# Performance work log

Hardware: AMD Instinct MI355X
Metric: run time of the kernel (lower is better)

Reference implementation:

```python
import jax, jax.numpy as jnp
import numpy as np

N_NODES = 50000
N_EDGES = 1600000
NODE_DIM = 16
EDGE_DIM = 16
PIPE_F = 4
HID = 64
L = 3


def _lin(k, fan_in, fan_out):
    kw, kb = jax.random.split(k)
    bound = 1.0 / np.sqrt(fan_in)
    w = jax.random.uniform(kw, (fan_in, fan_out), jnp.float32, -bound, bound)
    b = jax.random.uniform(kb, (fan_out,), jnp.float32, -bound, bound)
    return w, b


def setup_inputs() -> dict:
    key = jax.random.key(0)
    ks = jax.random.split(key, 16)
    leak_area = jax.random.normal(ks[0], (N_NODES, 1), jnp.float32)
    pipe_attrs = jax.random.normal(ks[1], (N_EDGES, PIPE_F), jnp.float32)
    edge_index = jax.random.randint(ks[2], (2, N_EDGES), 0, N_NODES, jnp.int32)
    node_embed_w, node_embed_b = _lin(ks[3], 1, NODE_DIM)
    edge_embed_w, edge_embed_b = _lin(ks[4], PIPE_F, EDGE_DIM)
    # per-layer MLP params, stacked along leading layer axis
    ew1, eb1, ew2, eb2, nw1, nb1, nw2, nb2 = [], [], [], [], [], [], [], []
    for l in range(L):
        kl = jax.random.fold_in(ks[5], l)
        k1, k2, k3, k4 = jax.random.split(kl, 4)
        w, b = _lin(k1, 2 * NODE_DIM + EDGE_DIM, HID); ew1.append(w); eb1.append(b)
        w, b = _lin(k2, HID, EDGE_DIM); ew2.append(w); eb2.append(b)
        w, b = _lin(k3, NODE_DIM + EDGE_DIM, HID); nw1.append(w); nb1.append(b)
        w, b = _lin(k4, HID, NODE_DIM); nw2.append(w); nb2.append(b)
    final_node_w, final_node_b = _lin(ks[6], NODE_DIM, 1)
    final_edge_w, final_edge_b = _lin(ks[7], EDGE_DIM, 1)
    return {
        "leak_area": leak_area,
        "pipe_attrs": pipe_attrs,
        "edge_index": edge_index,
        "node_embed_w": node_embed_w, "node_embed_b": node_embed_b,
        "edge_embed_w": edge_embed_w, "edge_embed_b": edge_embed_b,
        "edge_mlp_w1": jnp.stack(ew1), "edge_mlp_b1": jnp.stack(eb1),
        "edge_mlp_w2": jnp.stack(ew2), "edge_mlp_b2": jnp.stack(eb2),
        "node_mlp_w1": jnp.stack(nw1), "node_mlp_b1": jnp.stack(nb1),
        "node_mlp_w2": jnp.stack(nw2), "node_mlp_b2": jnp.stack(nb2),
        "final_node_w": final_node_w, "final_node_b": final_node_b,
        "final_edge_w": final_edge_w, "final_edge_b": final_edge_b,
    }


def reference(leak_area, pipe_attrs, edge_index,
              node_embed_w, node_embed_b, edge_embed_w, edge_embed_b,
              edge_mlp_w1, edge_mlp_b1, edge_mlp_w2, edge_mlp_b2,
              node_mlp_w1, node_mlp_b1, node_mlp_w2, node_mlp_b2,
              final_node_w, final_node_b, final_edge_w, final_edge_b):
    x = leak_area @ node_embed_w + node_embed_b          # [N, node_dim]
    e = pipe_attrs @ edge_embed_w + edge_embed_b          # [E, edge_dim]
    src = edge_index[0]  # x_j (source, PyG default flow source_to_target)
    dst = edge_index[1]  # x_i (target); aggregation index
    n = x.shape[0]
    num_layers = edge_mlp_w1.shape[0]
    ones = jnp.ones((src.shape[0], 1), x.dtype)
    deg = jax.ops.segment_sum(ones, dst, num_segments=n)  # [N,1]
    inv_deg = 1.0 / jnp.maximum(deg, 1.0)
    for l in range(num_layers):
        # message: small MLP on [x_i, x_j, e] per edge
        m_in = jnp.concatenate([x[dst], x[src], e], axis=-1)       # [E, 2d+de]
        h = jax.nn.relu(m_in @ edge_mlp_w1[l] + edge_mlp_b1[l])    # [E, 64]
        msg = h @ edge_mlp_w2[l] + edge_mlp_b2[l]                  # [E, de]
        # mean-aggregate to target nodes
        aggr = jax.ops.segment_sum(msg, dst, num_segments=n) * inv_deg  # [N, de]
        # node update MLP
        u_in = jnp.concatenate([x, aggr], axis=-1)                 # [N, d+de]
        x = jax.nn.relu(u_in @ node_mlp_w1[l] + node_mlp_b1[l]) @ node_mlp_w2[l] + node_mlp_b2[l]
    H = (x @ final_node_w + final_node_b)[:, 0]   # [N]
    q = (e @ final_edge_w + final_edge_b)[:, 0]   # [E]
    return H, q
```

## Files before the change

kernel.cpp:

```cpp
#include <hip/hip_runtime.h>
#include <hip/hip_bf16.h>

#define NN 50000
#define NE 1600000
#define NB 391
#define CBLK 392
#define EPB 4096

typedef __attribute__((ext_vector_type(8))) short bf16x8;
typedef __attribute__((ext_vector_type(4))) float f32x4;

#define B_HAG   0
#define B_QW    (B_HAG + NN*64*4)
#define B_NF    (B_QW + 32)
#define B_W1B   (B_NF + 3*8*64*8*2)
#define B_XB0   (B_W1B + 3*8*64*8*2)
#define B_XB1   (B_XB0 + NN*16*2)
#define B_EPK   (B_XB1 + NN*16*2)
#define B_OFF   (B_EPK + NE*16)
#define B_BCNT  (B_OFF + (NN+1)*4)
#define B_BASE  (B_BCNT + CBLK*NB*4)
#define B_GTOT  (B_BASE + (NB+1)*4)
#define B_END   (B_GTOT + NB*4)

static __device__ __forceinline__ unsigned short f2bf(float f) {
    union { __hip_bfloat16 h; unsigned short u; } cv;
    cv.h = __float2bfloat16(f);
    return cv.u;
}
static __device__ __forceinline__ unsigned pk2(float a, float b) {
    unsigned r;
    asm("v_cvt_pk_bf16_f32 %0, %1, %2" : "=v"(r) : "v"(a), "v"(b));
    return r;
}
static __device__ __forceinline__ float bf2f(unsigned short u) {
    return __uint_as_float((unsigned)u << 16);
}
static __device__ __forceinline__ bf16x8 mk8(unsigned a, unsigned b, unsigned c, unsigned d) {
    union { bf16x8 v; uint4 u; } cv;
    cv.u = make_uint4(a, b, c, d);
    return cv.v;
}

__global__ void prep_kernel(const float* __restrict__ ew1, const float* __restrict__ eb1,
                            const float* __restrict__ nw1, const float* __restrict__ ew2,
                            const float* __restrict__ nw2,
                            const float* __restrict__ eeW, const float* __restrict__ eeB,
                            const float* __restrict__ few, const float* __restrict__ feb,
                            unsigned short* __restrict__ w1b, unsigned short* __restrict__ nf,
                            float* __restrict__ qw)
{
    int t0 = blockIdx.x * blockDim.x + threadIdx.x;
    int stride = gridDim.x * blockDim.x;
    for (int idx = t0; idx < 3 * 8 * 64 * 8; idx += stride) {
        int l = idx >> 12;
        int r = idx & 4095;
        int f = r >> 9;
        int lane = (r >> 3) & 63;
        int e = r & 7;
        int col = lane & 15;
        int krow = ((lane >> 4) << 3) + e;
        {
            int tt = f >> 1, s = f & 1;
            int k = krow + (s << 5);
            int j = (tt << 4) + col;
            float v = 0.f;
            if (k < 32) {
                v = ew1[l * 3072 + k * 64 + j];
            } else if (k < 36) {
                int f2 = k - 32;
                float acc = 0.f;
                for (int m = 0; m < 16; m++) acc += eeW[f2 * 16 + m] * ew1[l * 3072 + (32 + m) * 64 + j];
                v = acc;
            } else if (k == 36) {
                float acc = eb1[l * 64 + j];
                for (int m = 0; m < 16; m++) acc += eeB[m] * ew1[l * 3072 + (32 + m) * 64 + j];
                v = acc;
            }
            w1b[idx] = f2bf(v);
        }
        {
            float v;
            if (f < 2)      v = ew2[l * 1024 + (f * 32 + krow) * 16 + col];
            else if (f < 6) v = nw1[l * 2048 + krow * 64 + (f - 2) * 16 + col];
            else            v = nw2[l * 1024 + ((f - 6) * 32 + krow) * 16 + col];
            nf[idx] = f2bf(v);
        }
    }
    if (t0 < 4) {
        float s = 0.f;
        for (int k = 0; k < 16; k++) s += eeW[t0 * 16 + k] * few[k];
        qw[t0] = s;
    } else if (t0 == 4) {
        float s = feb[0];
        for (int k = 0; k < 16; k++) s += eeB[k] * few[k];
        qw[4] = s;
    }
}

__global__ __launch_bounds__(256) void node_init_kernel(
    const float* __restrict__ leak, const float* __restrict__ nw, const float* __restrict__ nb,
    unsigned short* __restrict__ xb0, float* __restrict__ hag)
{
    int n = blockIdx.x * blockDim.x + threadIdx.x;
    if (n >= NN) return;
    float la = leak[n];
    float v[16];
    #pragma unroll
    for (int i = 0; i < 16; i++) v[i] = la * nw[i] + nb[i];
    unsigned pk[8];
    #pragma unroll
    for (int i = 0; i < 8; i++) pk[i] = pk2(v[2 * i], v[2 * i + 1]);
    uint4* xo = reinterpret_cast<uint4*>(xb0 + n * 16);
    xo[0] = make_uint4(pk[0], pk[1], pk[2], pk[3]);
    xo[1] = make_uint4(pk[4], pk[5], pk[6], pk[7]);
    float4 z = {0.f, 0.f, 0.f, 0.f};
    float4* hp = reinterpret_cast<float4*>(hag + n * 64);
    #pragma unroll
    for (int j = 0; j < 16; j++) hp[j] = z;
}

__global__ __launch_bounds__(1024) void bucket_count_kernel(
    const int* __restrict__ dst, int* __restrict__ bcnt)
{
    __shared__ int hist[NB];
    int t = threadIdx.x;
    for (int i = t; i < NB; i += 1024) hist[i] = 0;
    __syncthreads();
    int base = blockIdx.x * EPB;
    #pragma unroll
    for (int i = 0; i < 4; i++) {
        int idx = base + i * 1024 + t;
        if (idx < NE) atomicAdd(&hist[dst[idx] >> 7], 1);
    }
    __syncthreads();
    for (int i = t; i < NB; i += 1024) bcnt[blockIdx.x * NB + i] = hist[i];
}

__global__ __launch_bounds__(512) void scan_blocks_kernel(
    int* __restrict__ bcnt, int* __restrict__ gtot)
{
    __shared__ int sm[512];
    int b = blockIdx.x;
    int t = threadIdx.x;
    int v = (t < CBLK) ? bcnt[t * NB + b] : 0;
    sm[t] = v;
    __syncthreads();
    for (int o = 1; o < 512; o <<= 1) {
        int x = (t >= o) ? sm[t - o] : 0;
        __syncthreads();
        sm[t] += x;
        __syncthreads();
    }
    if (t < CBLK) bcnt[t * NB + b] = sm[t] - v;
    if (t == 511) gtot[b] = sm[511];
}

__global__ __launch_bounds__(512) void scan_top_kernel(
    const int* __restrict__ gtot, int* __restrict__ gbase)
{
    __shared__ int sm[512];
    int t = threadIdx.x;
    int v = (t < NB) ? gtot[t] : 0;
    sm[t] = v;
    __syncthreads();
    for (int o = 1; o < 512; o <<= 1) {
        int x = (t >= o) ? sm[t - o] : 0;
        __syncthreads();
        sm[t] += x;
        __syncthreads();
    }
    if (t < NB) gbase[t] = sm[t] - v;
    if (t == 0) gbase[NB] = NE;
}

__global__ __launch_bounds__(1024) void bucket_scatter_kernel(
    const int* __restrict__ ei, const float* __restrict__ pa,
    const int* __restrict__ bcnt, const int* __restrict__ gbase,
    const float* __restrict__ qw,
    float* __restrict__ qout, uint4* __restrict__ epk)
{
    __shared__ int hist[NB];
    int t = threadIdx.x;
    for (int i = t; i < NB; i += 1024) hist[i] = 0;
    __syncthreads();
    int base = blockIdx.x * EPB;
    #pragma unroll
    for (int i = 0; i < 4; i++) {
        int idx = base + i * 1024 + t;
        if (idx < NE) {
            int d = ei[NE + idx];
            int b = d >> 7;
            float4 p = reinterpret_cast<const float4*>(pa)[idx];
            qout[idx] = qw[4] + p.x * qw[0] + p.y * qw[1] + p.z * qw[2] + p.w * qw[3];
            int lr = atomicAdd(&hist[b], 1);
            int pos = gbase[b] + bcnt[blockIdx.x * NB + b] + lr;
            uint4 v;
            v.x = (unsigned)ei[idx];
            v.y = (unsigned)d;
            v.z = pk2(p.x, p.y);
            v.w = pk2(p.z, p.w);
            epk[pos] = v;
        }
    }
}

__global__ __launch_bounds__(1024) void fine_sort_kernel(
    const int* __restrict__ gbase, uint4* __restrict__ epk, int* __restrict__ off)
{
    __shared__ int hist[128];
    __shared__ int fb[128];
    int t = threadIdx.x;
    int b = blockIdx.x;
    int S = gbase[b], E = gbase[b + 1];
    if (t < 128) hist[t] = 0;
    __syncthreads();

    uint4 r[12];
    int lr[12];
    #pragma unroll
    for (int i = 0; i < 12; i++) {
        int gi = S + i * 1024 + t;
        if (gi < E) {
            r[i] = epk[gi];
            lr[i] = atomicAdd(&hist[(int)(r[i].y & 127u)], 1);
        }
    }
    __syncthreads();
    if (t < 128) fb[t] = hist[t];
    __syncthreads();
    for (int o = 1; o < 128; o <<= 1) {
        int v = 0;
        if (t < 128 && t >= o) v = fb[t - o];
        __syncthreads();
        if (t < 128) fb[t] += v;
        __syncthreads();
    }
    int d0 = b << 7;
    if (t < 128 && d0 + t < NN) off[d0 + t] = S + fb[t] - hist[t];
    if (b == NB - 1 && t == 0) off[NN] = NE;
    __syncthreads();
    #pragma unroll
    for (int i = 0; i < 12; i++) {
        int gi = S + i * 1024 + t;
        if (gi < E) {
            int fd = (int)(r[i].y & 127u);
            int pos = S + (fb[fd] - hist[fd]) + lr[i];
            epk[pos] = r[i];
        }
    }
}

__global__ __launch_bounds__(128, 5) void edge_mfma_kernel(
    const unsigned short* __restrict__ xb,
    const uint4* __restrict__ epk,
    const int* __restrict__ off,
    const unsigned short* __restrict__ w1b,
    float* __restrict__ hag)
{
    __shared__ unsigned short hbuf[2][64 * 68];
    int tid = threadIdx.x;
    int lane = tid & 63;
    int wid = tid >> 6;
    int wave = blockIdx.x * 2 + wid;
    int base = wave * 64;
    if (base >= NE) return;
    int ar = lane & 15;
    int ap = lane >> 4;
    unsigned short* hb = &hbuf[wid][0];

    uint4 ev0 = epk[base + 0  + ar];
    uint4 ev1 = epk[base + 16 + ar];
    uint4 ev2 = epk[base + 32 + ar];
    uint4 ev3 = epk[base + 48 + ar];

    int r0 = (ap < 2) ? (int)ev0.y : (int)ev0.x;
    int r1 = (ap < 2) ? (int)ev1.y : (int)ev1.x;
    int r2 = (ap < 2) ? (int)ev2.y : (int)ev2.x;
    int r3 = (ap < 2) ? (int)ev3.y : (int)ev3.x;
    int half = (ap & 1) * 8;
    bf16x8 a00 = *reinterpret_cast<const bf16x8*>(xb + (size_t)r0 * 16 + half);
    bf16x8 a01 = *reinterpret_cast<const bf16x8*>(xb + (size_t)r1 * 16 + half);
    bf16x8 a02 = *reinterpret_cast<const bf16x8*>(xb + (size_t)r2 * 16 + half);
    bf16x8 a03 = *reinterpret_cast<const bf16x8*>(xb + (size_t)r3 * 16 + half);

    int d0 = __builtin_amdgcn_readfirstlane((int)ev0.y);

    bf16x8 Bf[8];
    const bf16x8* w1v = reinterpret_cast<const bf16x8*>(w1b);
    #pragma unroll
    for (int i = 0; i < 8; i++) Bf[i] = w1v[i * 64 + lane];

#define DO_TILE(EV, A0, TILE) do {                                             \
    bf16x8 a1 = (bf16x8)0;                                                     \
    if (ap == 0) {                                                             \
        a1[0] = (short)(EV.z & 0xffffu);                                       \
        a1[1] = (short)(EV.z >> 16);                                           \
        a1[2] = (short)(EV.w & 0xffffu);                                       \
        a1[3] = (short)(EV.w >> 16);                                           \
        a1[4] = (short)0x3f80;                                                 \
    }                                                                          \
    f32x4 C0 = {0.f, 0.f, 0.f, 0.f}, C1 = C0, C2 = C0, C3 = C0;                \
    C0 = __builtin_amdgcn_mfma_f32_16x16x32_bf16(A0, Bf[0], C0, 0, 0, 0);      \
    C0 = __builtin_amdgcn_mfma_f32_16x16x32_bf16(a1, Bf[1], C0, 0, 0, 0);      \
    C1 = __builtin_amdgcn_mfma_f32_16x16x32_bf16(A0, Bf[2], C1, 0, 0, 0);      \
    C1 = __builtin_amdgcn_mfma_f32_16x16x32_bf16(a1, Bf[3], C1, 0, 0, 0);      \
    C2 = __builtin_amdgcn_mfma_f32_16x16x32_bf16(A0, Bf[4], C2, 0, 0, 0);      \
    C2 = __builtin_amdgcn_mfma_f32_16x16x32_bf16(a1, Bf[5], C2, 0, 0, 0);      \
    C3 = __builtin_amdgcn_mfma_f32_16x16x32_bf16(A0, Bf[6], C3, 0, 0, 0);      \
    C3 = __builtin_amdgcn_mfma_f32_16x16x32_bf16(a1, Bf[7], C3, 0, 0, 0);      \
    int eoff = TILE * 16 + ap * 4;                                             \
    {                                                                          \
        unsigned lov = pk2(fmaxf(C0[0], 0.f), fmaxf(C0[1], 0.f));              \
        unsigned hiv = pk2(fmaxf(C0[2], 0.f), fmaxf(C0[3], 0.f));              \
        *reinterpret_cast<uint2*>(hb + (0 * 16 + ar) * 68 + eoff) = make_uint2(lov, hiv); \
    }                                                                          \
    {                                                                          \
        unsigned lov = pk2(fmaxf(C1[0], 0.f), fmaxf(C1[1], 0.f));              \
        unsigned hiv = pk2(fmaxf(C1[2], 0.f), fmaxf(C1[3], 0.f));              \
        *reinterpret_cast<uint2*>(hb + (1 * 16 + ar) * 68 + eoff) = make_uint2(lov, hiv); \
    }                                                                          \
    {                                                                          \
        unsigned lov = pk2(fmaxf(C2[0], 0.f), fmaxf(C2[1], 0.f));              \
        unsigned hiv = pk2(fmaxf(C2[2], 0.f), fmaxf(C2[3], 0.f));              \
        *reinterpret_cast<uint2*>(hb + (2 * 16 + ar) * 68 + eoff) = make_uint2(lov, hiv); \
    }                                                                          \
    {                                                                          \
        unsigned lov = pk2(fmaxf(C3[0], 0.f), fmaxf(C3[1], 0.f));              \
        unsigned hiv = pk2(fmaxf(C3[2], 0.f), fmaxf(C3[3], 0.f));              \
        *reinterpret_cast<uint2*>(hb + (3 * 16 + ar) * 68 + eoff) = make_uint2(lov, hiv); \
    }                                                                          \
} while (0)

    DO_TILE(ev0, a00, 0);
    DO_TILE(ev1, a01, 1);
    DO_TILE(ev2, a02, 2);
    DO_TILE(ev3, a03, 3);
#undef DO_TILE

    asm volatile("s_waitcnt lgkmcnt(0)" ::: "memory");
    __builtin_amdgcn_sched_barrier(0);

    int d = d0;
    int e = base;
    const int lim = base + 64;
    const unsigned short* hr = hb + lane * 68;
    while (e < lim) {
        int segend = off[d + 1];
        int eend = segend < lim ? segend : lim;
        float acc = 0.f;
        int i = e - base, iend = eend - base;
        for (; (i & 3) != 0 && i < iend; ++i) acc += bf2f(hr[i]);
        for (; i + 4 <= iend; i += 4) {
            uint2 u = *reinterpret_cast<const uint2*>(hr + i);
            acc += __uint_as_float(u.x << 16) + __uint_as_float(u.x & 0xffff0000u)
                 + __uint_as_float(u.y << 16) + __uint_as_float(u.y & 0xffff0000u);
        }
        for (; i < iend; ++i) acc += bf2f(hr[i]);
        unsafeAtomicAdd(&hag[(size_t)d * 64 + lane], acc);
        e = eend;
        if (segend <= lim) ++d;
    }
}

__global__ __launch_bounds__(256) void node_mfma_kernel(
    const unsigned short* __restrict__ xb, unsigned short* __restrict__ xbn,
    float* __restrict__ hag, const int* __restrict__ off,
    const unsigned short* __restrict__ nf,
    const float* __restrict__ eb2,
    const float* __restrict__ nb1, const float* __restrict__ nb2,
    const float* __restrict__ fnw, const float* __restrict__ fnb,
    float* __restrict__ Hout, int writeH)
{
    __shared__ unsigned short aggt[4][16 * 16];
    __shared__ unsigned short ht[4][16 * 64];
    __shared__ float ot[4][16 * 16];
    int tid = threadIdx.x;
    int lane = tid & 63;
    int wid = tid >> 6;
    int wave = blockIdx.x * 4 + wid;
    int n0 = wave * 16;
    if (n0 >= NN) return;
    int nr = lane & 15;
    int ap = lane >> 4;

    bf16x8 Bf[8];
    const bf16x8* nfv = reinterpret_cast<const bf16x8*>(nf);
    #pragma unroll
    for (int i = 0; i < 8; i++) Bf[i] = nfv[i * 64 + lane];

    float* hrow = hag + (size_t)(n0 + nr) * 64 + ap * 8;
    float4* h0p = reinterpret_cast<float4*>(hrow);
    float4* h1p = reinterpret_cast<float4*>(hrow + 32);
    float4 ha = h0p[0], hc = h0p[1];
    float4 he = h1p[0], hg = h1p[1];
    float4 z = {0.f, 0.f, 0.f, 0.f};
    h0p[0] = z; h0p[1] = z; h1p[0] = z; h1p[1] = z;
    bf16x8 agA0 = mk8(pk2(ha.x, ha.y), pk2(ha.z, ha.w), pk2(hc.x, hc.y), pk2(hc.z, hc.w));
    bf16x8 agA1 = mk8(pk2(he.x, he.y), pk2(he.z, he.w), pk2(hg.x, hg.y), pk2(hg.z, hg.w));
    f32x4 Cag = {0.f, 0.f, 0.f, 0.f};
    Cag = __builtin_amdgcn_mfma_f32_16x16x32_bf16(agA0, Bf[0], Cag, 0, 0, 0);
    Cag = __builtin_amdgcn_mfma_f32_16x16x32_bf16(agA1, Bf[1], Cag, 0, 0, 0);

    int bn = n0 + ap * 4;
    int o0 = off[bn], o1 = off[bn + 1], o2 = off[bn + 2], o3 = off[bn + 3], o4 = off[bn + 4];
    float ebv = eb2[nr];
    {
        int dgs[4] = {o1 - o0, o2 - o1, o3 - o2, o4 - o3};
        #pragma unroll
        for (int r = 0; r < 4; r++) {
            float inv = 1.0f / (float)(dgs[r] > 0 ? dgs[r] : 1);
            float val = Cag[r] * inv + ((dgs[r] > 0) ? ebv : 0.f);
            aggt[wid][(ap * 4 + r) * 16 + nr] = f2bf(val);
        }
    }
    asm volatile("s_waitcnt lgkmcnt(0)" ::: "memory");
    __builtin_amdgcn_sched_barrier(0);

    bf16x8 uA;
    if (ap < 2) uA = *reinterpret_cast<const bf16x8*>(xb + (size_t)(n0 + nr) * 16 + ap * 8);
    else        uA = *reinterpret_cast<const bf16x8*>(&aggt[wid][nr * 16 + (ap - 2) * 8]);

    f32x4 Ch0 = {0.f, 0.f, 0.f, 0.f}, Ch1 = Ch0, Ch2 = Ch0, Ch3 = Ch0;
    Ch0 = __builtin_amdgcn_mfma_f32_16x16x32_bf16(uA, Bf[2], Ch0, 0, 0, 0);
    Ch1 = __builtin_amdgcn_mfma_f32_16x16x32_bf16(uA, Bf[3], Ch1, 0, 0, 0);
    Ch2 = __builtin_amdgcn_mfma_f32_16x16x32_bf16(uA, Bf[4], Ch2, 0, 0, 0);
    Ch3 = __builtin_amdgcn_mfma_f32_16x16x32_bf16(uA, Bf[5], Ch3, 0, 0, 0);

#define H_EPI(C, TT) do {                                                      \
    int j = (TT) * 16 + nr;                                                    \
    float bv = nb1[j];                                                         \
    _Pragma("unroll")                                                          \
    for (int r = 0; r < 4; r++) {                                              \
        float h = fmaxf(C[r] + bv, 0.f);                                       \
        ht[wid][(ap * 4 + r) * 64 + j] = f2bf(h);                              \
    }                                                                          \
} while (0)
    H_EPI(Ch0, 0); H_EPI(Ch1, 1); H_EPI(Ch2, 2); H_EPI(Ch3, 3);
#undef H_EPI

    asm volatile("s_waitcnt lgkmcnt(0)" ::: "memory");
    __builtin_amdgcn_sched_barrier(0);

    bf16x8 hA0 = *reinterpret_cast<const bf16x8*>(&ht[wid][nr * 64 + ap * 8]);
    bf16x8 hA1 = *reinterpret_cast<const bf16x8*>(&ht[wid][nr * 64 + 32 + ap * 8]);
    f32x4 Co = {0.f, 0.f, 0.f, 0.f};
    Co = __builtin_amdgcn_mfma_f32_16x16x32_bf16(hA0, Bf[6], Co, 0, 0, 0);
    Co = __builtin_amdgcn_mfma_f32_16x16x32_bf16(hA1, Bf[7], Co, 0, 0, 0);
    {
        float bv = nb2[nr];
        #pragma unroll
        for (int r = 0; r < 4; r++) ot[wid][(ap * 4 + r) * 16 + nr] = Co[r] + bv;
    }
    asm volatile("s_waitcnt lgkmcnt(0)" ::: "memory");
    __builtin_amdgcn_sched_barrier(0);

    if (lane < 16) {
        const float* orow = &ot[wid][lane * 16];
        float o[16];
        #pragma unroll
        for (int k = 0; k < 16; k++) o[k] = orow[k];
        unsigned pk[8];
        #pragma unroll
        for (int i = 0; i < 8; i++) pk[i] = pk2(o[2 * i], o[2 * i + 1]);
        uint4* xo = reinterpret_cast<uint4*>(xbn + (size_t)(n0 + lane) * 16);
        xo[0] = make_uint4(pk[0], pk[1], pk[2], pk[3]);
        xo[1] = make_uint4(pk[4], pk[5], pk[6], pk[7]);
        if (writeH) {
            float s = fnb[0];
            #pragma unroll
            for (int k = 0; k < 16; k++) s += o[k] * fnw[k];
            Hout[n0 + lane] = s;
        }
    }
}

extern "C" void kernel_launch(void* const* d_in, const int* in_sizes, int n_in,
                              void* d_out, int out_size, void* d_ws, size_t ws_size,
                              hipStream_t stream)
{
    const float* leak = (const float*)d_in[0];
    const float* pa   = (const float*)d_in[1];
    const int*   ei   = (const int*)d_in[2];
    const float* neww = (const float*)d_in[3];
    const float* newb = (const float*)d_in[4];
    const float* eeW  = (const float*)d_in[5];
    const float* eeB  = (const float*)d_in[6];
    const float* ew1  = (const float*)d_in[7];
    const float* eb1  = (const float*)d_in[8];
    const float* ew2  = (const float*)d_in[9];
    const float* eb2  = (const float*)d_in[10];
    const float* nw1  = (const float*)d_in[11];
    const float* nb1  = (const float*)d_in[12];
    const float* nw2  = (const float*)d_in[13];
    const float* nb2  = (const float*)d_in[14];
    const float* fnw  = (const float*)d_in[15];
    const float* fnb  = (const float*)d_in[16];
    const float* few  = (const float*)d_in[17];
    const float* feb  = (const float*)d_in[18];

    char* wsb = (char*)d_ws;
    float*          hag   = (float*)(wsb + B_HAG);
    float*          qw    = (float*)(wsb + B_QW);
    unsigned short* nf    = (unsigned short*)(wsb + B_NF);
    unsigned short* w1b   = (unsigned short*)(wsb + B_W1B);
    unsigned short* xb0   = (unsigned short*)(wsb + B_XB0);
    unsigned short* xb1   = (unsigned short*)(wsb + B_XB1);
    uint4*          epk   = (uint4*)(wsb + B_EPK);
    int*            off   = (int*)(wsb + B_OFF);
    int*            bcnt  = (int*)(wsb + B_BCNT);
    int*            gbase = (int*)(wsb + B_BASE);
    int*            gtot  = (int*)(wsb + B_GTOT);

    float* H = (float*)d_out;
    float* q = (float*)d_out + NN;
    const int* dstp = ei + NE;

    prep_kernel<<<16, 256, 0, stream>>>(ew1, eb1, nw1, ew2, nw2, eeW, eeB, few, feb,
                                        w1b, nf, qw);
    node_init_kernel<<<(NN + 255) / 256, 256, 0, stream>>>(leak, neww, newb, xb0, hag);
    bucket_count_kernel<<<CBLK, 1024, 0, stream>>>(dstp, bcnt);
    scan_blocks_kernel<<<NB, 512, 0, stream>>>(bcnt, gtot);
    scan_top_kernel<<<1, 512, 0, stream>>>(gtot, gbase);
    bucket_scatter_kernel<<<CBLK, 1024, 0, stream>>>(ei, pa, bcnt, gbase, qw, q, epk);
    fine_sort_kernel<<<NB, 1024, 0, stream>>>(gbase, epk, off);

    int nwaves = NN / 16;
    int nblocks = (nwaves + 3) / 4;

    unsigned short* xcur = xb0;
    unsigned short* xnxt = xb1;
    for (int l = 0; l < 3; l++) {
        edge_mfma_kernel<<<NE / 128, 128, 0, stream>>>(
            xcur, epk, off, w1b + l * 4096, hag);
        node_mfma_kernel<<<nblocks, 256, 0, stream>>>(
            xcur, xnxt, hag, off, nf + l * 4096, eb2 + l * 16,
            nb1 + l * 64, nb2 + l * 16, fnw, fnb, H, (l == 2) ? 1 : 0);
        unsigned short* tmp = xcur; xcur = xnxt; xnxt = tmp;
    }
}
```

Before: 200.7 us.

## Accumulate edge hidden activations in registers per destination run, drop LDS staging

The edge kernel no longer writes ReLU'd hidden activations to a shared-memory buffer and then walks CSR offsets to reduce them. Each lane now accumulates its MFMA outputs in registers while the destination stays the same, and flushes with atomics to the node accumulator whenever the destination changes. This removes the LDS write/read round trip and the off[] lookups. The cost is that the partial sums are no longer rounded to bf16, and lanes whose runs break at different points may issue more atomics. Block size goes to 256 threads with 3 blocks per CU, and the sort and scatter kernels are restructured so all loads are issued before the LDS atomics, to expose memory-level parallelism.

Result: slower. 565.2 us (+181.6%).

```diff
diff --git a/kernel.cpp b/kernel.cpp
--- a/kernel.cpp
+++ b/kernel.cpp
@@ -32,9 +32,6 @@
     unsigned r;
     asm("v_cvt_pk_bf16_f32 %0, %1, %2" : "=v"(r) : "v"(a), "v"(b));
     return r;
-}
-static __device__ __forceinline__ float bf2f(unsigned short u) {
-    return __uint_as_float((unsigned)u << 16);
 }
 static __device__ __forceinline__ bf16x8 mk8(unsigned a, unsigned b, unsigned c, unsigned d) {
     union { bf16x8 v; uint4 u; } cv;
@@ -128,11 +125,15 @@
     for (int i = t; i < NB; i += 1024) hist[i] = 0;
     __syncthreads();
     int base = blockIdx.x * EPB;
+    int b[4];
     #pragma unroll
     for (int i = 0; i < 4; i++) {
         int idx = base + i * 1024 + t;
-        if (idx < NE) atomicAdd(&hist[dst[idx] >> 7], 1);
-    }
+        b[i] = (idx < NE) ? (dst[idx] >> 7) : -1;
+    }
+    #pragma unroll
+    for (int i = 0; i < 4; i++)
+        if (b[i] >= 0) atomicAdd(&hist[b[i]], 1);
     __syncthreads();
     for (int i = t; i < NB; i += 1024) bcnt[blockIdx.x * NB + i] = hist[i];
 }
@@ -185,24 +186,47 @@
     for (int i = t; i < NB; i += 1024) hist[i] = 0;
     __syncthreads();
     int base = blockIdx.x * EPB;
+    float q0 = qw[0], q1 = qw[1], q2 = qw[2], q3 = qw[3], q4 = qw[4];
+    int d[4], s[4];
+    float4 p[4];
     #pragma unroll
     for (int i = 0; i < 4; i++) {
         int idx = base + i * 1024 + t;
         if (idx < NE) {
-            int d = ei[NE + idx];
-            int b = d >> 7;
-            float4 p = reinterpret_cast<const float4*>(pa)[idx];
-            qout[idx] = qw[4] + p.x * qw[0] + p.y * qw[1] + p.z * qw[2] + p.w * qw[3];
-            int lr = atomicAdd(&hist[b], 1);
-            int pos = gbase[b] + bcnt[blockIdx.x * NB + b] + lr;
+            d[i] = ei[NE + idx];
+            s[i] = ei[idx];
+            p[i] = reinterpret_cast<const float4*>(pa)[idx];
+        } else {
+            d[i] = -1;
+        }
+    }
+    #pragma unroll
+    for (int i = 0; i < 4; i++) {
+        int idx = base + i * 1024 + t;
+        if (d[i] >= 0)
+            qout[idx] = q4 + p[i].x * q0 + p[i].y * q1 + p[i].z * q2 + p[i].w * q3;
+    }
+    int lr[4];
+    #pragma unroll
+    for (int i = 0; i < 4; i++)
+        if (d[i] >= 0) lr[i] = atomicAdd(&hist[d[i] >> 7], 1);
+    int bs[4];
+    #pragma unroll
+    for (int i = 0; i < 4; i++)
+        if (d[i] >= 0) {
+            int b = d[i] >> 7;
+            bs[i] = gbase[b] + bcnt[blockIdx.x * NB + b];
+        }
+    #pragma unroll
+    for (int i = 0; i < 4; i++)
+        if (d[i] >= 0) {
             uint4 v;
-            v.x = (unsigned)ei[idx];
-            v.y = (unsigned)d;
-            v.z = pk2(p.x, p.y);
-            v.w = pk2(p.z, p.w);
-            epk[pos] = v;
-        }
-    }
+            v.x = (unsigned)s[i];
+            v.y = (unsigned)d[i];
+            v.z = pk2(p[i].x, p[i].y);
+            v.w = pk2(p[i].z, p[i].w);
+            epk[bs[i] + lr[i]] = v;
+        }
 }
 
 __global__ __launch_bounds__(1024) void fine_sort_kernel(
@@ -217,14 +241,16 @@
     __syncthreads();
 
     uint4 r[12];
-    int lr[12];
     #pragma unroll
     for (int i = 0; i < 12; i++) {
         int gi = S + i * 1024 + t;
-        if (gi < E) {
-            r[i] = epk[gi];
-            lr[i] = atomicAdd(&hist[(int)(r[i].y & 127u)], 1);
-        }
+        if (gi < E) r[i] = epk[gi];
+    }
+    int lr[12];
+    #pragma unroll
+    for (int i = 0; i < 12; i++) {
+        int gi = S + i * 1024 + t;
+        if (gi < E) lr[i] = atomicAdd(&hist[(int)(r[i].y & 127u)], 1);
     }
     __syncthreads();
     if (t < 128) fb[t] = hist[t];
@@ -251,28 +277,33 @@
     }
 }
 
-__global__ __launch_bounds__(128, 5) void edge_mfma_kernel(
+__global__ __launch_bounds__(256, 3) void edge_mfma_kernel(
     const unsigned short* __restrict__ xb,
     const uint4* __restrict__ epk,
-    const int* __restrict__ off,
     const unsigned short* __restrict__ w1b,
     float* __restrict__ hag)
 {
-    __shared__ unsigned short hbuf[2][64 * 68];
+    __shared__ int sdst[4][64];
     int tid = threadIdx.x;
     int lane = tid & 63;
     int wid = tid >> 6;
-    int wave = blockIdx.x * 2 + wid;
+    int wave = blockIdx.x * 4 + wid;
     int base = wave * 64;
     if (base >= NE) return;
     int ar = lane & 15;
     int ap = lane >> 4;
-    unsigned short* hb = &hbuf[wid][0];
 
     uint4 ev0 = epk[base + 0  + ar];
     uint4 ev1 = epk[base + 16 + ar];
     uint4 ev2 = epk[base + 32 + ar];
     uint4 ev3 = epk[base + 48 + ar];
+
+    if (ap == 0) {
+        sdst[wid][0  + ar] = (int)ev0.y;
+        sdst[wid][16 + ar] = (int)ev1.y;
+        sdst[wid][32 + ar] = (int)ev2.y;
+        sdst[wid][48 + ar] = (int)ev3.y;
+    }
 
     int r0 = (ap < 2) ? (int)ev0.y : (int)ev0.x;
     int r1 = (ap < 2) ? (int)ev1.y : (int)ev1.x;
@@ -284,14 +315,43 @@
     bf16x8 a02 = *reinterpret_cast<const bf16x8*>(xb + (size_t)r2 * 16 + half);
     bf16x8 a03 = *reinterpret_cast<const bf16x8*>(xb + (size_t)r3 * 16 + half);
 
-    int d0 = __builtin_amdgcn_readfirstlane((int)ev0.y);
-
     bf16x8 Bf[8];
     const bf16x8* w1v = reinterpret_cast<const bf16x8*>(w1b);
     #pragma unroll
     for (int i = 0; i < 8; i++) Bf[i] = w1v[i * 64 + lane];
 
-#define DO_TILE(EV, A0, TILE) do {                                             \
+    asm volatile("s_waitcnt lgkmcnt(0)" ::: "memory");
+    __builtin_amdgcn_sched_barrier(0);
+
+    int4 sd0 = *reinterpret_cast<const int4*>(&sdst[wid][0  + ap * 4]);
+    int4 sd1 = *reinterpret_cast<const int4*>(&sdst[wid][16 + ap * 4]);
+    int4 sd2 = *reinterpret_cast<const int4*>(&sdst[wid][32 + ap * 4]);
+    int4 sd3 = *reinterpret_cast<const int4*>(&sdst[wid][48 + ap * 4]);
+
+    float ac0 = 0.f, ac1 = 0.f, ac2 = 0.f, ac3 = 0.f;
+    int cur = sd0.x;
+
+#define FLUSH() do {                                                           \
+    unsafeAtomicAdd(&hag[(size_t)cur * 64 +      ar], ac0);                    \
+    unsafeAtomicAdd(&hag[(size_t)cur * 64 + 16 + ar], ac1);                    \
+    unsafeAtomicAdd(&hag[(size_t)cur * 64 + 32 + ar], ac2);                    \
+    unsafeAtomicAdd(&hag[(size_t)cur * 64 + 48 + ar], ac3);                    \
+} while (0)
+
+#define EPI(DT, V0, V1, V2, V3) do {                                           \
+    int dt_ = (DT);                                                            \
+    if (dt_ != cur) {                                                          \
+        FLUSH();                                                               \
+        ac0 = 0.f; ac1 = 0.f; ac2 = 0.f; ac3 = 0.f;                            \
+        cur = dt_;                                                             \
+    }                                                                          \
+    ac0 += fmaxf(V0, 0.f);                                                     \
+    ac1 += fmaxf(V1, 0.f);                                                     \
+    ac2 += fmaxf(V2, 0.f);                                                     \
+    ac3 += fmaxf(V3, 0.f);                                                     \
+} while (0)
+
+#define DO_TILE(EV, A0, SD) do {                                               \
     bf16x8 a1 = (bf16x8)0;                                                     \
     if (ap == 0) {                                                             \
         a1[0] = (short)(EV.z & 0xffffu);                                       \
@@ -309,58 +369,20 @@
     C2 = __builtin_amdgcn_mfma_f32_16x16x32_bf16(a1, Bf[5], C2, 0, 0, 0);      \
     C3 = __builtin_amdgcn_mfma_f32_16x16x32_bf16(A0, Bf[6], C3, 0, 0, 0);      \
     C3 = __builtin_amdgcn_mfma_f32_16x16x32_bf16(a1, Bf[7], C3, 0, 0, 0);      \
-    int eoff = TILE * 16 + ap * 4;                                             \
-    {                                                                          \
-        unsigned lov = pk2(fmaxf(C0[0], 0.f), fmaxf(C0[1], 0.f));              \
-        unsigned hiv = pk2(fmaxf(C0[2], 0.f), fmaxf(C0[3], 0.f));              \
-        *reinterpret_cast<uint2*>(hb + (0 * 16 + ar) * 68 + eoff) = make_uint2(lov, hiv); \
-    }                                                                          \
-    {                                                                          \
-        unsigned lov = pk2(fmaxf(C1[0], 0.f), fmaxf(C1[1], 0.f));              \
-        unsigned hiv = pk2(fmaxf(C1[2], 0.f), fmaxf(C1[3], 0.f));              \
-        *reinterpret_cast<uint2*>(hb + (1 * 16 + ar) * 68 + eoff) = make_uint2(lov, hiv); \
-    }                                                                          \
-    {                                                                          \
-        unsigned lov = pk2(fmaxf(C2[0], 0.f), fmaxf(C2[1], 0.f));              \
-        unsigned hiv = pk2(fmaxf(C2[2], 0.f), fmaxf(C2[3], 0.f));              \
-        *reinterpret_cast<uint2*>(hb + (2 * 16 + ar) * 68 + eoff) = make_uint2(lov, hiv); \
-    }                                                                          \
-    {                                                                          \
-        unsigned lov = pk2(fmaxf(C3[0], 0.f), fmaxf(C3[1], 0.f));              \
-        unsigned hiv = pk2(fmaxf(C3[2], 0.f), fmaxf(C3[3], 0.f));              \
-        *reinterpret_cast<uint2*>(hb + (3 * 16 + ar) * 68 + eoff) = make_uint2(lov, hiv); \
-    }                                                                          \
+    EPI(SD.x, C0[0], C1[0], C2[0], C3[0]);                                     \
+    EPI(SD.y, C0[1], C1[1], C2[1], C3[1]);                                     \
+    EPI(SD.z, C0[2], C1[2], C2[2], C3[2]);                                     \
+    EPI(SD.w, C0[3], C1[3], C2[3], C3[3]);                                     \
 } while (0)
 
-    DO_TILE(ev0, a00, 0);
-    DO_TILE(ev1, a01, 1);
-    DO_TILE(ev2, a02, 2);
-    DO_TILE(ev3, a03, 3);
+    DO_TILE(ev0, a00, sd0);
+    DO_TILE(ev1, a01, sd1);
+    DO_TILE(ev2, a02, sd2);
+    DO_TILE(ev3, a03, sd3);
+    FLUSH();
 #undef DO_TILE
-
-    asm volatile("s_waitcnt lgkmcnt(0)" ::: "memory");
-    __builtin_amdgcn_sched_barrier(0);
-
-    int d = d0;
-    int e = base;
-    const int lim = base + 64;
-    const unsigned short* hr = hb + lane * 68;
-    while (e < lim) {
-        int segend = off[d + 1];
-        int eend = segend < lim ? segend : lim;
-        float acc = 0.f;
-        int i = e - base, iend = eend - base;
-        for (; (i & 3) != 0 && i < iend; ++i) acc += bf2f(hr[i]);
-        for (; i + 4 <= iend; i += 4) {
-            uint2 u = *reinterpret_cast<const uint2*>(hr + i);
-            acc += __uint_as_float(u.x << 16) + __uint_as_float(u.x & 0xffff0000u)
-                 + __uint_as_float(u.y << 16) + __uint_as_float(u.y & 0xffff0000u);
-        }
-        for (; i < iend; ++i) acc += bf2f(hr[i]);
-        unsafeAtomicAdd(&hag[(size_t)d * 64 + lane], acc);
-        e = eend;
-        if (segend <= lim) ++d;
-    }
+#undef EPI
+#undef FLUSH
 }
 
 __global__ __launch_bounds__(256) void node_mfma_kernel(
@@ -531,8 +553,8 @@
     unsigned short* xcur = xb0;
     unsigned short* xnxt = xb1;
     for (int l = 0; l < 3; l++) {
-        edge_mfma_kernel<<<NE / 128, 128, 0, stream>>>(
-            xcur, epk, off, w1b + l * 4096, hag);
+        edge_mfma_kernel<<<NE / 256, 256, 0, stream>>>(
+            xcur, epk, w1b + l * 4096, hag);
         node_mfma_kernel<<<nblocks, 256, 0, stream>>>(
             xcur, xnxt, hag, off, nf + l * 4096, eb2 + l * 16,
             nb1 + l * 64, nb2 + l * 16, fnw, fnb, H, (l == 2) ? 1 : 0);
```
